# Optimization experiments

Hardware: AMD Instinct MI355X
Metric: run time of the kernel (lower is better)

## Reference

```python
import jax, jax.numpy as jnp
import numpy as np

N = 50000
E = 500000
IN_DIM = 128
HID = 128
EDGE_DIM = 1
MAX_DEPTH = 4  # depth values in [0, MAX_DEPTH]


def setup_inputs() -> dict:
    key = jax.random.key(0)
    ks = jax.random.split(key, 10)
    x = jax.random.normal(ks[0], (N, IN_DIM), jnp.float32)
    edge_index = jax.random.randint(ks[1], (2, E), 0, N)
    edge_attr = jax.random.normal(ks[2], (E, EDGE_DIM), jnp.float32)
    depth = jax.random.randint(ks[3], (N,), 0, MAX_DEPTH + 1)
    def w(k, sh):
        return (jax.random.normal(k, sh, jnp.float32) / np.float32(np.sqrt(sh[0])))
    return {
        "x": x, "edge_index": edge_index, "edge_attr": edge_attr, "depth": depth,
        "pw": w(ks[4], (IN_DIM, HID)), "pb": jnp.zeros((HID,), jnp.float32),
        "mw1": w(ks[5], (HID + EDGE_DIM, HID)), "mb1": jnp.zeros((HID,), jnp.float32),
        "mw2": w(ks[6], (HID, HID)), "mb2": jnp.zeros((HID,), jnp.float32),
        "uw1": w(ks[7], (2 * HID, HID)), "ub1": jnp.zeros((HID,), jnp.float32),
        "uw2": w(ks[8], (HID, HID)), "ub2": jnp.zeros((HID,), jnp.float32),
    }


def reference(x, edge_index, edge_attr, depth, pw, pb, mw1, mb1, mw2, mb2, uw1, ub1, uw2, ub2):
    src, dst = edge_index[0], edge_index[1]
    dst_depth = depth[dst]  # [E]
    h = x @ pw + pb  # node_proj -> [N, HID]
    # Sequential topological DP over depth levels (static unroll, small count).
    for d in range(1, MAX_DEPTH + 1):
        emask = dst_depth == d  # [E]
        # msg_mlp over all edges using current h (lower-depth nodes already updated)
        msg_in = jnp.concatenate([h[src], edge_attr], axis=-1)  # [E, HID+EDGE_DIM]
        msgs = jax.nn.relu(jax.nn.relu(msg_in @ mw1 + mb1) @ mw2 + mb2)
        msgs = jnp.where(emask[:, None], msgs, jnp.zeros((), h.dtype))
        agg = jax.ops.segment_sum(msgs, dst, num_segments=N)  # [N, HID]
        counts = jax.ops.segment_sum(emask.astype(h.dtype), dst, num_segments=N)
        agg = agg / jnp.clip(counts, 1.0)[:, None]  # mean aggregation, clamp(min=1)
        upd_in = jnp.concatenate([h, agg], axis=-1)  # [N, 2*HID]
        h_new = jax.nn.relu(jax.nn.relu(upd_in @ uw1 + ub1) @ uw2 + ub2)
        h = jnp.where((depth == d)[:, None], h_new, h)
    return h
```

## Files before the change

### kernel.cpp

```cpp
#include <hip/hip_runtime.h>

typedef _Float16 f16;
typedef f16 f16x2 __attribute__((ext_vector_type(2)));
typedef f16 f16x8 __attribute__((ext_vector_type(8)));
typedef float f32x4 __attribute__((ext_vector_type(4)));
typedef float f32x2 __attribute__((ext_vector_type(2)));

#define MFMA16(a, b, c) __builtin_amdgcn_mfma_f32_16x16x32_f16((a), (b), (c), 0, 0, 0)

static __device__ __forceinline__ f16x8 cvt8(const float* __restrict__ p) {
    f32x4 p0 = *(const f32x4*)p;
    f32x4 p1 = *(const f32x4*)(p + 4);
    f16x8 a;
    a[0] = (f16)p0[0]; a[1] = (f16)p0[1]; a[2] = (f16)p0[2]; a[3] = (f16)p0[3];
    a[4] = (f16)p1[0]; a[5] = (f16)p1[1]; a[6] = (f16)p1[2]; a[7] = (f16)p1[3];
    return a;
}

__global__ __launch_bounds__(256) void k_prep(
        const float* __restrict__ pw, const float* __restrict__ mw1,
        const float* __restrict__ mw2, const float* __restrict__ uw1,
        const float* __restrict__ uw2,
        f16* __restrict__ pwp, f16* __restrict__ mw1p, f16* __restrict__ mw2p,
        f16* __restrict__ uw1p, f16* __restrict__ uw2p,
        const int* __restrict__ ei, int* __restrict__ degv,
        const int* __restrict__ dep, int* __restrict__ dcnt,
        int4* __restrict__ recs, int CB, int E, int N) {
    __shared__ int lcnt[4];
    __shared__ int lbase[4];
    int b = blockIdx.x;
    int t = threadIdx.x;
    if (b < 48) {
        const float* W; f16* out; int fb;
        if (b < 8)       { W = pw;  out = pwp;  fb = b; }
        else if (b < 16) { W = mw1; out = mw1p; fb = b - 8; }
        else if (b < 24) { W = mw2; out = mw2p; fb = b - 16; }
        else if (b < 40) { W = uw1; out = uw1p; fb = b - 24; }
        else             { W = uw2; out = uw2p; fb = b - 40; }
        int idx = fb * 256 + t;
        int lane = idx & 63;
        int nt = (idx >> 6) & 7;
        int kt = idx >> 9;
        int colx = lane & 15, quad = lane >> 4;
        f16* o = out + (size_t)idx * 8;
        const float* wb = W + (size_t)(kt * 32 + quad * 8) * 128 + nt * 16 + colx;
#pragma unroll
        for (int j = 0; j < 8; j++) o[j] = (f16)wb[(size_t)j * 128];
    } else if (b < 48 + CB) {
        int e = (b - 48) * 256 + t;
        if (e < E) atomicAdd(&degv[ei[E + e]], 1);
    } else {
        if (t < 4) lcnt[t] = 0;
        __syncthreads();
        int v = (b - 48 - CB) * 256 + t;
        int d = (v < N) ? dep[v] : 0;
        int p = -1;
        if (d >= 1 && d <= 4) p = atomicAdd(&lcnt[d - 1], 1);
        __syncthreads();
        if (t < 4) lbase[t] = (lcnt[t] > 0) ? atomicAdd(&dcnt[t], lcnt[t]) : 0;
        __syncthreads();
        if (d >= 1 && d <= 4) recs[(size_t)(d - 1) * N + lbase[d - 1] + p].x = v;
    }
}

__global__ __launch_bounds__(256) void k_mid(
        const int* __restrict__ degv, int* __restrict__ bsum, int SB,
        const float* __restrict__ x, const f16* __restrict__ pwp,
        const f16* __restrict__ mw1p, const float* __restrict__ pb,
        const float* __restrict__ mb1, float* __restrict__ h,
        f16* __restrict__ hh, f16* __restrict__ t, int N) {
    __shared__ __align__(16) f16 lds[4][16 * 136];
    __shared__ int wsum[4];
    int tid = threadIdx.x;
    if ((int)blockIdx.x < SB) {
        int idx = blockIdx.x * 256 + tid;
        int v = (idx < N) ? degv[idx] : 0;
#pragma unroll
        for (int off = 32; off; off >>= 1) v += __shfl_down(v, off, 64);
        if ((tid & 63) == 0) wsum[tid >> 6] = v;
        __syncthreads();
        if (tid == 0) bsum[blockIdx.x] = wsum[0] + wsum[1] + wsum[2] + wsum[3];
        return;
    }
    int lane = tid & 63, w = tid >> 6;
    int colx = lane & 15, quad = lane >> 4;
    int base = ((blockIdx.x - SB) * 4 + w) * 16;
    int arow = base + colx;
    int u = arow < N ? arow : N - 1;

    f32x4 c1[8];
#pragma unroll
    for (int nt = 0; nt < 8; nt++) c1[nt] = (f32x4){0.f, 0.f, 0.f, 0.f};
#pragma unroll
    for (int kt = 0; kt < 4; kt++) {
        f16x8 a = cvt8(x + (size_t)u * 128 + kt * 32 + quad * 8);
#pragma unroll
        for (int nt = 0; nt < 8; nt++) {
            f16x8 b = *(const f16x8*)(pwp + ((size_t)(kt * 8 + nt) * 64 + lane) * 8);
            c1[nt] = MFMA16(a, b, c1[nt]);
        }
    }
#pragma unroll
    for (int nt = 0; nt < 8; nt++) {
        float bias = pb[nt * 16 + colx];
#pragma unroll
        for (int reg = 0; reg < 4; reg++) {
            int row = quad * 4 + reg;
            int node = base + row;
            float v = c1[nt][reg] + bias;
            lds[w][row * 136 + nt * 16 + colx] = (f16)v;
            if (node < N) {
                h[(size_t)node * 128 + nt * 16 + colx] = v;
                hh[(size_t)node * 128 + nt * 16 + colx] = (f16)v;
            }
        }
    }
    f32x4 c2[8];
#pragma unroll
    for (int nt = 0; nt < 8; nt++) c2[nt] = (f32x4){0.f, 0.f, 0.f, 0.f};
#pragma unroll
    for (int kt = 0; kt < 4; kt++) {
        f16x8 a = *(const f16x8*)&lds[w][colx * 136 + kt * 32 + quad * 8];
#pragma unroll
        for (int nt = 0; nt < 8; nt++) {
            f16x8 b = *(const f16x8*)(mw1p + ((size_t)(kt * 8 + nt) * 64 + lane) * 8);
            c2[nt] = MFMA16(a, b, c2[nt]);
        }
    }
#pragma unroll
    for (int nt = 0; nt < 8; nt++) {
        float bias = mb1[nt * 16 + colx];
#pragma unroll
        for (int reg = 0; reg < 4; reg++) {
            int node = base + quad * 4 + reg;
            if (node < N) t[(size_t)node * 128 + nt * 16 + colx] = (f16)(c2[nt][reg] + bias);
        }
    }
}

__global__ __launch_bounds__(256) void k_scanC(const int* __restrict__ degv,
                                               const int* __restrict__ bsum,
                                               int* __restrict__ rowp, int N, int E) {
    __shared__ int lds[256];
    __shared__ int wo[4];
    int b = blockIdx.x, t = threadIdx.x;
    int idx = b * 256 + t;
    int v = (idx < N) ? degv[idx] : 0;
    lds[t] = v;
    __syncthreads();
#pragma unroll
    for (int d = 1; d < 256; d <<= 1) {
        int u = (t >= d) ? lds[t - d] : 0;
        __syncthreads();
        lds[t] += u;
        __syncthreads();
    }
    int off = 0;
    for (int j = t; j < b; j += 256) off += bsum[j];
#pragma unroll
    for (int o = 32; o; o >>= 1) off += __shfl_down(off, o, 64);
    if ((t & 63) == 0) wo[t >> 6] = off;
    __syncthreads();
    int boff = wo[0] + wo[1] + wo[2] + wo[3];
    if (idx < N) rowp[idx] = boff + lds[t] - v;
    if (b == 0 && t == 0) rowp[N] = E;
}

__global__ __launch_bounds__(256) void k_scat(const int* __restrict__ ei,
                                              const float* __restrict__ eattr,
                                              const int* __restrict__ dep,
                                              const int* __restrict__ rowp,
                                              int* __restrict__ cur,
                                              int2* __restrict__ esea,
                                              int4* __restrict__ recs,
                                              const int* __restrict__ dcnt,
                                              int E, int N) {
    int gtid = blockIdx.x * 256 + threadIdx.x;
    int gsz = gridDim.x * 256;
    for (int e = gtid; e < E; e += gsz) {
        int s = ei[e], d = ei[E + e];
        int p = rowp[d] + atomicAdd(&cur[d], 1);
        esea[p] = (int2){s | (dep[s] << 20), __float_as_int(eattr[e])};
    }
    for (int d4 = 0; d4 < 4; d4++) {
        int cnt = dcnt[d4];
        for (int i = gtid; i < cnt; i += gsz) {
            int4* r = &recs[(size_t)d4 * N + i];
            int u = r->x;
            r->y = rowp[u];
            r->z = rowp[u + 1];
        }
    }
}

__global__ __launch_bounds__(512) void k_md(
        const f16* __restrict__ tOrg, f16* __restrict__ tUpd,
        const float* __restrict__ mw1, const float* __restrict__ mb2,
        const f16* __restrict__ mw2p, const int2* __restrict__ esea,
        const int4* __restrict__ recs, const int* __restrict__ dcnt,
        const f16* __restrict__ hh, const f16* __restrict__ uw1p,
        const f16* __restrict__ uw2p, const f16* __restrict__ mw1p,
        const float* __restrict__ ub1, const float* __restrict__ ub2,
        const float* __restrict__ mb1, float* __restrict__ h,
        int dIdx, int N) {
    __shared__ __align__(16) f16 bsm[128 * 128];
    __shared__ __align__(16) f16 tbuf[8][16][136];
    __shared__ __align__(16) f16 pool[16][136];
    __shared__ __align__(16) f16 sout[16][136];
    __shared__ int2 ebuf[8][16];
    __shared__ int ids[16], se0[16], se1[16];
    f16* hbuf = &tbuf[0][0][0];

    const int tid = threadIdx.x;
    const int lane = tid & 63;
    const int w = tid >> 6;
    const int colx = lane & 15, quad = lane >> 4;
    const int cnt = dcnt[dIdx];

    {
        const f16x8* s8 = (const f16x8*)mw2p;
        f16x8* d8 = (f16x8*)bsm;
#pragma unroll
        for (int i = 0; i < 4; i++) d8[i * 512 + tid] = s8[i * 512 + tid];
    }

    const float* w1r = mw1 + 128 * 128;
    f16x8 w1h[4];
#pragma unroll
    for (int kt = 0; kt < 4; kt++) {
        f32x4 q0 = *(const f32x4*)(w1r + kt * 32 + quad * 8);
        f32x4 q1 = *(const f32x4*)(w1r + kt * 32 + quad * 8 + 4);
        w1h[kt][0] = (f16)q0[0]; w1h[kt][1] = (f16)q0[1];
        w1h[kt][2] = (f16)q0[2]; w1h[kt][3] = (f16)q0[3];
        w1h[kt][4] = (f16)q1[0]; w1h[kt][5] = (f16)q1[1];
        w1h[kt][6] = (f16)q1[2]; w1h[kt][7] = (f16)q1[3];
    }
    float mb2v[8];
#pragma unroll
    for (int nt = 0; nt < 8; nt++) mb2v[nt] = mb2[nt * 16 + colx];

    const int b = blockIdx.x, nb = gridDim.x;
    const int s0 = (int)((long long)cnt * b / nb);
    const int s1 = (int)((long long)cnt * (b + 1) / nb);

    auto srow = [&](int sv) -> const f16* {
        const f16* tb = ((unsigned)((sv >> 20) - 1) < (unsigned)dIdx) ? tUpd : tOrg;
        return tb + (size_t)(sv & 0xFFFFF) * 128;
    };

    __syncthreads();

    for (int cs = s0; cs < s1; cs += 16) {
        int cc = s1 - cs; if (cc > 16) cc = 16;
        if (tid < 16) {
            if (tid < cc) {
                int4 r = recs[(size_t)dIdx * N + cs + tid];
                ids[tid] = r.x; se0[tid] = r.y; se1[tid] = r.z;
            } else {
                ids[tid] = 0; se0[tid] = 0; se1[tid] = 0;
            }
        }
        __syncthreads();

        for (int g = 0; g < 2; g++) {
            int maxT = 0;
#pragma unroll
            for (int s = 0; s < 8; s++) {
                int r = g * 8 + s;
                int tc = (se1[r] - se0[r] + 15) >> 4;
                if (tc > maxT) maxT = tc;
            }
            float aggv[8] = {0.f, 0.f, 0.f, 0.f, 0.f, 0.f, 0.f, 0.f};
            for (int rd = 0; rd < maxT; rd++) {
                if (tid < 128) {
                    int s = tid >> 4, j = tid & 15;
                    int r = g * 8 + s;
                    int es = se0[r] + rd * 16 + j;
                    if (es < se1[r]) ebuf[s][j] = esea[es];
                }
                __syncthreads();
#pragma unroll
                for (int it = 0; it < 4; it++) {
                    int task = it * 512 + tid;
                    int row = task >> 4, seg = task & 15;
                    int s = row >> 4, j = row & 15;
                    int r = g * 8 + s;
                    int es = se0[r] + rd * 16 + j;
                    if (es < se1[r]) {
                        int sv = ebuf[s][j].x;
                        *(f16x8*)&tbuf[s][j][seg * 8] =
                            *(const f16x8*)(srow(sv) + seg * 8);
                    }
                }
                __syncthreads();
                {
                    int r = g * 8 + w;
                    int bs = se0[r] + rd * 16;
                    int rem = se1[r] - bs;
                    if (rem > 0) {
                        f16 eah = (f16)__int_as_float(ebuf[w][colx].y);
                        f16x8 afr[4];
#pragma unroll
                        for (int kt = 0; kt < 4; kt++) {
                            f16x8 v = *(const f16x8*)&tbuf[w][colx][kt * 32 + quad * 8];
                            f16x8 o;
#pragma unroll
                            for (int j2 = 0; j2 < 8; j2++) {
                                f16 qv = v[j2] + eah * w1h[kt][j2];
                                o[j2] = qv > (f16)0 ? qv : (f16)0;
                            }
                            afr[kt] = o;
                        }
#pragma unroll
                        for (int nt = 0; nt < 8; nt++) {
                            f32x4 c = (f32x4){0.f, 0.f, 0.f, 0.f};
#pragma unroll
                            for (int kt = 0; kt < 4; kt++) {
                                f16x8 bb = *(const f16x8*)&bsm[((kt * 8 + nt) * 64 + lane) * 8];
                                c = MFMA16(afr[kt], bb, c);
                            }
#pragma unroll
                            for (int reg = 0; reg < 4; reg++)
                                if (quad * 4 + reg < rem)
                                    aggv[nt] += fmaxf(c[reg] + mb2v[nt], 0.f);
                        }
                    }
                }
                __syncthreads();
            }
            {
                int r = g * 8 + w;
                int deg = se1[r] - se0[r];
                float inv = 1.f / (float)(deg > 1 ? deg : 1);
#pragma unroll
                for (int nt = 0; nt < 8; nt++) {
                    float s = aggv[nt];
                    s += __shfl_xor(s, 16, 64);
                    s += __shfl_xor(s, 32, 64);
                    if (quad == 0) pool[r][nt * 16 + colx] = (f16)(s * inv);
                }
            }
        }
        __syncthreads();

        if (tid < 256) {
            int row = tid >> 4, seg = tid & 15;
            *(f16x8*)&hbuf[row * 136 + seg * 8] =
                *(const f16x8*)(hh + (size_t)ids[row] * 128 + seg * 8);
        }
        __syncthreads();

        f32x4 c1 = (f32x4){0.f, 0.f, 0.f, 0.f};
#pragma unroll
        for (int kt = 0; kt < 8; kt++) {
            f16x8 a;
            if (kt < 4)
                a = *(const f16x8*)&hbuf[colx * 136 + kt * 32 + quad * 8];
            else
                a = *(const f16x8*)&pool[colx][(kt - 4) * 32 + quad * 8];
            f16x8 bb = *(const f16x8*)(uw1p + ((size_t)(kt * 8 + w) * 64 + lane) * 8);
            c1 = MFMA16(a, bb, c1);
        }
        {
            float bias = ub1[w * 16 + colx];
#pragma unroll
            for (int reg = 0; reg < 4; reg++) {
                int row = quad * 4 + reg;
                sout[row][w * 16 + colx] = (f16)fmaxf(c1[reg] + bias, 0.f);
            }
        }
        __syncthreads();
        f32x4 c2 = (f32x4){0.f, 0.f, 0.f, 0.f};
#pragma unroll
        for (int kt = 0; kt < 4; kt++) {
            f16x8 a = *(const f16x8*)&sout[colx][kt * 32 + quad * 8];
            f16x8 bb = *(const f16x8*)(uw2p + ((size_t)(kt * 8 + w) * 64 + lane) * 8);
            c2 = MFMA16(a, bb, c2);
        }
        {
            float bias = ub2[w * 16 + colx];
#pragma unroll
            for (int reg = 0; reg < 4; reg++) {
                int row = quad * 4 + reg;
                float v = fmaxf(c2[reg] + bias, 0.f);
                pool[row][w * 16 + colx] = (f16)v;
                if (row < cc)
                    h[(size_t)ids[row] * 128 + w * 16 + colx] = v;
            }
        }
        __syncthreads();
        if (dIdx < 3) {
            f32x4 c3 = (f32x4){0.f, 0.f, 0.f, 0.f};
#pragma unroll
            for (int kt = 0; kt < 4; kt++) {
                f16x8 a = *(const f16x8*)&pool[colx][kt * 32 + quad * 8];
                f16x8 bb = *(const f16x8*)(mw1p + ((size_t)(kt * 8 + w) * 64 + lane) * 8);
                c3 = MFMA16(a, bb, c3);
            }
            float bias = mb1[w * 16 + colx];
#pragma unroll
            for (int reg = 0; reg < 4; reg++) {
                int row = quad * 4 + reg;
                if (row < cc)
                    tUpd[(size_t)ids[row] * 128 + w * 16 + colx] =
                        (f16)(c3[reg] + bias);
            }
        }
        __syncthreads();
    }
}

extern "C" void kernel_launch(void* const* d_in, const int* in_sizes, int n_in,
                              void* d_out, int out_size, void* d_ws, size_t ws_size,
                              hipStream_t stream) {
    const float* x    = (const float*)d_in[0];
    const int*   ei   = (const int*)d_in[1];
    const float* eatt = (const float*)d_in[2];
    const int*   dep  = (const int*)d_in[3];
    const float* pw   = (const float*)d_in[4];
    const float* pb   = (const float*)d_in[5];
    const float* mw1  = (const float*)d_in[6];
    const float* mb1  = (const float*)d_in[7];
    const float* mw2  = (const float*)d_in[8];
    const float* mb2  = (const float*)d_in[9];
    const float* uw1  = (const float*)d_in[10];
    const float* ub1  = (const float*)d_in[11];
    const float* uw2  = (const float*)d_in[12];
    const float* ub2  = (const float*)d_in[13];
    float* h = (float*)d_out;

    int N = in_sizes[3];
    int E = in_sizes[1] / 2;
    int NB = (N + 255) / 256;
    int CB = (E + 255) / 256;

    char* ws = (char*)d_ws;
    size_t o = 0;
    auto alloc = [&](size_t bytes) -> char* {
        char* p = ws + o;
        o += (bytes + 255) & ~(size_t)255;
        return p;
    };
    f16*   t    = (f16*)alloc((size_t)N * 128 * 2);
    f16*   hh   = (f16*)alloc((size_t)N * 128 * 2);
    f16*   tUpd = (f16*)alloc((size_t)N * 128 * 2);
    char*  z0   = (char*)alloc(0);
    int*   degv = (int*)alloc((size_t)N * 4);
    int*   cur  = (int*)alloc((size_t)N * 4);
    int*   dcnt = (int*)alloc(64);
    size_t zbytes = (size_t)((char*)alloc(0) - z0);
    int*   rowp = (int*)alloc((size_t)(N + 1) * 4);
    int*   bsum = (int*)alloc((size_t)NB * 4);
    int2*  esea = (int2*)alloc((size_t)E * 8);
    int4*  recs = (int4*)alloc((size_t)4 * N * 16);
    f16*   pwp  = (f16*)alloc(128 * 128 * 2);
    f16*   mw1p = (f16*)alloc(128 * 128 * 2);
    f16*   mw2p = (f16*)alloc(128 * 128 * 2);
    f16*   uw1p = (f16*)alloc(256 * 128 * 2);
    f16*   uw2p = (f16*)alloc(128 * 128 * 2);

    hipMemsetAsync(z0, 0, zbytes, stream);

    k_prep<<<48 + CB + NB, 256, 0, stream>>>(pw, mw1, mw2, uw1, uw2,
                                             pwp, mw1p, mw2p, uw1p, uw2p,
                                             ei, degv, dep, dcnt, recs, CB, E, N);
    int PB = (N + 63) / 64;
    k_mid<<<NB + PB, 256, 0, stream>>>(degv, bsum, NB, x, pwp, mw1p, pb, mb1,
                                       h, hh, t, N);
    k_scanC<<<NB, 256, 0, stream>>>(degv, bsum, rowp, N, E);
    k_scat<<<CB, 256, 0, stream>>>(ei, eatt, dep, rowp, cur, esea, recs, dcnt, E, N);

    for (int d = 0; d < 4; d++) {
        k_md<<<512, 512, 0, stream>>>(t, tUpd, mw1, mb2, mw2p, esea, recs, dcnt,
                                      hh, uw1p, uw2p, mw1p, ub1, ub2, mb1, h,
                                      d, N);
    }
}
```

Measured before the change: 345.7 us.

## Precompute per-edge first-layer messages via source-ordered CSR before MLP

Adds a source-sorted CSR (out-degree counts, scan, forward edge list) and a new per-level k_msg kernel. For each source node it reads the projected row once and writes the relu(t + ea*w) message for every outgoing edge into a dst-ordered message buffer. The destination CSR is now ordered by depth-sorted node, so each level's edges form a contiguous range. k_md then streams precomputed messages contiguously instead of gathering random source rows and applying the edge-attr FMA itself. The trade is an extra kernel launch per level and a large E×128 f16 scratch buffer written and read each level.

```diff
diff --git a/kernel.cpp b/kernel.cpp
--- a/kernel.cpp
+++ b/kernel.cpp
@@ -17,13 +17,25 @@
     return a;
 }
 
+static __device__ __forceinline__ int sorted_node(int i, const int* __restrict__ dcnt,
+                                                  const int4* __restrict__ recs, int N) {
+    int o1 = dcnt[0], o2 = o1 + dcnt[1], o3 = o2 + dcnt[2], o4 = o3 + dcnt[3];
+    int dI, off;
+    if (i < o1)      { dI = 0; off = 0; }
+    else if (i < o2) { dI = 1; off = o1; }
+    else if (i < o3) { dI = 2; off = o2; }
+    else if (i < o4) { dI = 3; off = o3; }
+    else return -1;
+    return recs[(size_t)dI * N + (i - off)].x;
+}
+
 __global__ __launch_bounds__(256) void k_prep(
         const float* __restrict__ pw, const float* __restrict__ mw1,
         const float* __restrict__ mw2, const float* __restrict__ uw1,
         const float* __restrict__ uw2,
         f16* __restrict__ pwp, f16* __restrict__ mw1p, f16* __restrict__ mw2p,
         f16* __restrict__ uw1p, f16* __restrict__ uw2p,
-        const int* __restrict__ ei, int* __restrict__ degv,
+        const int* __restrict__ ei, int* __restrict__ degv, int* __restrict__ odeg,
         const int* __restrict__ dep, int* __restrict__ dcnt,
         int4* __restrict__ recs, int CB, int E, int N) {
     __shared__ int lcnt[4];
@@ -48,7 +60,10 @@
         for (int j = 0; j < 8; j++) o[j] = (f16)wb[(size_t)j * 128];
     } else if (b < 48 + CB) {
         int e = (b - 48) * 256 + t;
-        if (e < E) atomicAdd(&degv[ei[E + e]], 1);
+        if (e < E) {
+            atomicAdd(&degv[ei[E + e]], 1);
+            atomicAdd(&odeg[ei[e]], 1);
+        }
     } else {
         if (t < 4) lcnt[t] = 0;
         __syncthreads();
@@ -64,7 +79,9 @@
 }
 
 __global__ __launch_bounds__(256) void k_mid(
-        const int* __restrict__ degv, int* __restrict__ bsum, int SB,
+        const int* __restrict__ degv, const int* __restrict__ odeg,
+        const int4* __restrict__ recs, const int* __restrict__ dcnt,
+        int* __restrict__ bsum, int SB,
         const float* __restrict__ x, const f16* __restrict__ pwp,
         const f16* __restrict__ mw1p, const float* __restrict__ pb,
         const float* __restrict__ mb1, float* __restrict__ h,
@@ -72,19 +89,27 @@
     __shared__ __align__(16) f16 lds[4][16 * 136];
     __shared__ int wsum[4];
     int tid = threadIdx.x;
-    if ((int)blockIdx.x < SB) {
-        int idx = blockIdx.x * 256 + tid;
-        int v = (idx < N) ? degv[idx] : 0;
+    if ((int)blockIdx.x < 2 * SB) {
+        int bb = blockIdx.x;
+        int v = 0;
+        if (bb < SB) {
+            int i = bb * 256 + tid;
+            int node = sorted_node(i, dcnt, recs, N);
+            if (node >= 0) v = degv[node];
+        } else {
+            int i = (bb - SB) * 256 + tid;
+            v = (i < N) ? odeg[i] : 0;
+        }
 #pragma unroll
         for (int off = 32; off; off >>= 1) v += __shfl_down(v, off, 64);
         if ((tid & 63) == 0) wsum[tid >> 6] = v;
         __syncthreads();
-        if (tid == 0) bsum[blockIdx.x] = wsum[0] + wsum[1] + wsum[2] + wsum[3];
+        if (tid == 0) bsum[bb] = wsum[0] + wsum[1] + wsum[2] + wsum[3];
         return;
     }
     int lane = tid & 63, w = tid >> 6;
     int colx = lane & 15, quad = lane >> 4;
-    int base = ((blockIdx.x - SB) * 4 + w) * 16;
+    int base = ((blockIdx.x - 2 * SB) * 4 + w) * 16;
     int arow = base + colx;
     int u = arow < N ? arow : N - 1;
 
@@ -138,14 +163,31 @@
     }
 }
 
-__global__ __launch_bounds__(256) void k_scanC(const int* __restrict__ degv,
-                                               const int* __restrict__ bsum,
-                                               int* __restrict__ rowp, int N, int E) {
+__global__ __launch_bounds__(256) void k_scanC(
+        const int* __restrict__ degv, const int* __restrict__ odeg,
+        int4* __restrict__ recs, const int* __restrict__ dcnt,
+        const int* __restrict__ bsum, int* __restrict__ rowp,
+        int* __restrict__ orowp, int NBv, int N, int E) {
     __shared__ int lds[256];
     __shared__ int wo[4];
     int b = blockIdx.x, t = threadIdx.x;
-    int idx = b * 256 + t;
-    int v = (idx < N) ? degv[idx] : 0;
+    bool isSrc = b >= NBv;
+    int i = (isSrc ? b - NBv : b) * 256 + t;
+    int node = -1, dI = -1, joff = 0;
+    int v = 0;
+    if (!isSrc) {
+        int o1 = dcnt[0], o2 = o1 + dcnt[1], o3 = o2 + dcnt[2], o4 = o3 + dcnt[3];
+        if (i < o1)      { dI = 0; joff = 0; }
+        else if (i < o2) { dI = 1; joff = o1; }
+        else if (i < o3) { dI = 2; joff = o2; }
+        else if (i < o4) { dI = 3; joff = o3; }
+        if (dI >= 0) {
+            node = recs[(size_t)dI * N + (i - joff)].x;
+            v = degv[node];
+        }
+    } else {
+        v = (i < N) ? odeg[i] : 0;
+    }
     lds[t] = v;
     __syncthreads();
 #pragma unroll
@@ -156,58 +198,94 @@
         __syncthreads();
     }
     int off = 0;
-    for (int j = t; j < b; j += 256) off += bsum[j];
+    for (int j = (isSrc ? NBv : 0) + t; j < b; j += 256) off += bsum[j];
 #pragma unroll
     for (int o = 32; o; o >>= 1) off += __shfl_down(off, o, 64);
     if ((t & 63) == 0) wo[t >> 6] = off;
     __syncthreads();
     int boff = wo[0] + wo[1] + wo[2] + wo[3];
-    if (idx < N) rowp[idx] = boff + lds[t] - v;
-    if (b == 0 && t == 0) rowp[N] = E;
+    int val = boff + lds[t] - v;
+    if (!isSrc && dI >= 0) {
+        rowp[node] = val;
+        int4* r = &recs[(size_t)dI * N + (i - joff)];
+        r->y = val;
+        r->z = val + v;
+    }
+    if (isSrc && i < N) orowp[i] = val;
+    if (isSrc && b == NBv && t == 0) orowp[N] = E;
 }
 
 __global__ __launch_bounds__(256) void k_scat(const int* __restrict__ ei,
                                               const float* __restrict__ eattr,
                                               const int* __restrict__ dep,
                                               const int* __restrict__ rowp,
+                                              const int* __restrict__ orowp,
                                               int* __restrict__ cur,
-                                              int2* __restrict__ esea,
-                                              int4* __restrict__ recs,
-                                              const int* __restrict__ dcnt,
+                                              int* __restrict__ ocur,
+                                              int2* __restrict__ fwd,
                                               int E, int N) {
     int gtid = blockIdx.x * 256 + threadIdx.x;
     int gsz = gridDim.x * 256;
     for (int e = gtid; e < E; e += gsz) {
-        int s = ei[e], d = ei[E + e];
-        int p = rowp[d] + atomicAdd(&cur[d], 1);
-        esea[p] = (int2){s | (dep[s] << 20), __float_as_int(eattr[e])};
-    }
-    for (int d4 = 0; d4 < 4; d4++) {
-        int cnt = dcnt[d4];
-        for (int i = gtid; i < cnt; i += gsz) {
-            int4* r = &recs[(size_t)d4 * N + i];
-            int u = r->x;
-            r->y = rowp[u];
-            r->z = rowp[u + 1];
+        int s = ei[e], dn = ei[E + e];
+        int dd = dep[dn];
+        int px = -1;
+        if (dd >= 1) {
+            int p = rowp[dn] + atomicAdd(&cur[dn], 1);
+            px = p | (dd << 24);
+        }
+        int q = orowp[s] + atomicAdd(&ocur[s], 1);
+        fwd[q] = (int2){px, __float_as_int(eattr[e])};
+    }
+}
+
+__global__ __launch_bounds__(256) void k_msg(
+        const f16* __restrict__ tOrg, const f16* __restrict__ tUpd,
+        const float* __restrict__ mw1, const int* __restrict__ dep,
+        const int* __restrict__ orowp, const int2* __restrict__ fwd,
+        f16* __restrict__ msgbuf, int dIdx, int N) {
+    const int lane = threadIdx.x & 63;
+    const int gw = blockIdx.x * 4 + (threadIdx.x >> 6);
+    const int nw = gridDim.x * 4;
+    const float* w1r = mw1 + 128 * 128;
+    f32x2 wq = *(const f32x2*)(w1r + lane * 2);
+    f16 w0 = (f16)wq[0], w1 = (f16)wq[1];
+    const int want = dIdx + 1;
+
+    for (int s = gw; s < N; s += nw) {
+        int q0 = orowp[s], q1 = orowp[s + 1];
+        if (q0 == q1) continue;
+        int ds = dep[s];
+        const f16* tb = ((unsigned)(ds - 1) < (unsigned)dIdx) ? tUpd : tOrg;
+        f16x2 tv = *(const f16x2*)(tb + (size_t)s * 128 + lane * 2);
+        for (int q = q0; q < q1; q++) {
+            int2 f = fwd[q];
+            if (f.x >= 0 && (f.x >> 24) == want) {
+                f16 ea = (f16)__int_as_float(f.y);
+                f16 a0 = tv[0] + ea * w0;
+                f16 a1 = tv[1] + ea * w1;
+                a0 = a0 > (f16)0 ? a0 : (f16)0;
+                a1 = a1 > (f16)0 ? a1 : (f16)0;
+                f16x2 a = {a0, a1};
+                *(f16x2*)(msgbuf + (size_t)(f.x & 0xFFFFFF) * 128 + lane * 2) = a;
+            }
         }
     }
 }
 
 __global__ __launch_bounds__(512) void k_md(
-        const f16* __restrict__ tOrg, f16* __restrict__ tUpd,
-        const float* __restrict__ mw1, const float* __restrict__ mb2,
-        const f16* __restrict__ mw2p, const int2* __restrict__ esea,
+        const f16* __restrict__ msgbuf, const float* __restrict__ mb2,
+        const f16* __restrict__ mw2p,
         const int4* __restrict__ recs, const int* __restrict__ dcnt,
         const f16* __restrict__ hh, const f16* __restrict__ uw1p,
         const f16* __restrict__ uw2p, const f16* __restrict__ mw1p,
         const float* __restrict__ ub1, const float* __restrict__ ub2,
         const float* __restrict__ mb1, float* __restrict__ h,
-        int dIdx, int N) {
+        f16* __restrict__ tUpd, int dIdx, int N) {
     __shared__ __align__(16) f16 bsm[128 * 128];
     __shared__ __align__(16) f16 tbuf[8][16][136];
     __shared__ __align__(16) f16 pool[16][136];
     __shared__ __align__(16) f16 sout[16][136];
-    __shared__ int2 ebuf[8][16];
     __shared__ int ids[16], se0[16], se1[16];
     f16* hbuf = &tbuf[0][0][0];
 
@@ -223,18 +301,6 @@
 #pragma unroll
         for (int i = 0; i < 4; i++) d8[i * 512 + tid] = s8[i * 512 + tid];
     }
-
-    const float* w1r = mw1 + 128 * 128;
-    f16x8 w1h[4];
-#pragma unroll
-    for (int kt = 0; kt < 4; kt++) {
-        f32x4 q0 = *(const f32x4*)(w1r + kt * 32 + quad * 8);
-        f32x4 q1 = *(const f32x4*)(w1r + kt * 32 + quad * 8 + 4);
-        w1h[kt][0] = (f16)q0[0]; w1h[kt][1] = (f16)q0[1];
-        w1h[kt][2] = (f16)q0[2]; w1h[kt][3] = (f16)q0[3];
-        w1h[kt][4] = (f16)q1[0]; w1h[kt][5] = (f16)q1[1];
-        w1h[kt][6] = (f16)q1[2]; w1h[kt][7] = (f16)q1[3];
-    }
     float mb2v[8];
 #pragma unroll
     for (int nt = 0; nt < 8; nt++) mb2v[nt] = mb2[nt * 16 + colx];
@@ -242,11 +308,6 @@
     const int b = blockIdx.x, nb = gridDim.x;
     const int s0 = (int)((long long)cnt * b / nb);
     const int s1 = (int)((long long)cnt * (b + 1) / nb);
-
-    auto srow = [&](int sv) -> const f16* {
-        const f16* tb = ((unsigned)((sv >> 20) - 1) < (unsigned)dIdx) ? tUpd : tOrg;
-        return tb + (size_t)(sv & 0xFFFFF) * 128;
-    };
 
     __syncthreads();
 
@@ -272,13 +333,6 @@
             }
             float aggv[8] = {0.f, 0.f, 0.f, 0.f, 0.f, 0.f, 0.f, 0.f};
             for (int rd = 0; rd < maxT; rd++) {
-                if (tid < 128) {
-                    int s = tid >> 4, j = tid & 15;
-                    int r = g * 8 + s;
-                    int es = se0[r] + rd * 16 + j;
-                    if (es < se1[r]) ebuf[s][j] = esea[es];
-                }
-                __syncthreads();
 #pragma unroll
                 for (int it = 0; it < 4; it++) {
                     int task = it * 512 + tid;
@@ -287,9 +341,8 @@
                     int r = g * 8 + s;
                     int es = se0[r] + rd * 16 + j;
                     if (es < se1[r]) {
-                        int sv = ebuf[s][j].x;
                         *(f16x8*)&tbuf[s][j][seg * 8] =
-                            *(const f16x8*)(srow(sv) + seg * 8);
+                            *(const f16x8*)(msgbuf + (size_t)es * 128 + seg * 8);
                     }
                 }
                 __syncthreads();
@@ -298,19 +351,10 @@
                     int bs = se0[r] + rd * 16;
                     int rem = se1[r] - bs;
                     if (rem > 0) {
-                        f16 eah = (f16)__int_as_float(ebuf[w][colx].y);
                         f16x8 afr[4];
 #pragma unroll
-                        for (int kt = 0; kt < 4; kt++) {
-                            f16x8 v = *(const f16x8*)&tbuf[w][colx][kt * 32 + quad * 8];
-                            f16x8 o;
-#pragma unroll
-                            for (int j2 = 0; j2 < 8; j2++) {
-                                f16 qv = v[j2] + eah * w1h[kt][j2];
-                                o[j2] = qv > (f16)0 ? qv : (f16)0;
-                            }
-                            afr[kt] = o;
-                        }
+                        for (int kt = 0; kt < 4; kt++)
+                            afr[kt] = *(const f16x8*)&tbuf[w][colx][kt * 32 + quad * 8];
 #pragma unroll
                         for (int nt = 0; nt < 8; nt++) {
                             f32x4 c = (f32x4){0.f, 0.f, 0.f, 0.f};
@@ -446,33 +490,42 @@
     f16*   tUpd = (f16*)alloc((size_t)N * 128 * 2);
     char*  z0   = (char*)alloc(0);
     int*   degv = (int*)alloc((size_t)N * 4);
+    int*   odeg = (int*)alloc((size_t)N * 4);
     int*   cur  = (int*)alloc((size_t)N * 4);
+    int*   ocur = (int*)alloc((size_t)N * 4);
     int*   dcnt = (int*)alloc(64);
     size_t zbytes = (size_t)((char*)alloc(0) - z0);
-    int*   rowp = (int*)alloc((size_t)(N + 1) * 4);
-    int*   bsum = (int*)alloc((size_t)NB * 4);
-    int2*  esea = (int2*)alloc((size_t)E * 8);
-    int4*  recs = (int4*)alloc((size_t)4 * N * 16);
+    int*   rowp  = (int*)alloc((size_t)(N + 1) * 4);
+    int*   orowp = (int*)alloc((size_t)(N + 1) * 4);
+    int*   bsum  = (int*)alloc((size_t)2 * NB * 4);
+    int2*  fwd   = (int2*)alloc((size_t)E * 8);
+    int4*  recs  = (int4*)alloc((size_t)4 * N * 16);
     f16*   pwp  = (f16*)alloc(128 * 128 * 2);
     f16*   mw1p = (f16*)alloc(128 * 128 * 2);
     f16*   mw2p = (f16*)alloc(128 * 128 * 2);
     f16*   uw1p = (f16*)alloc(256 * 128 * 2);
     f16*   uw2p = (f16*)alloc(128 * 128 * 2);
+    f16*   msgbuf = (f16*)alloc((size_t)E * 128 * 2 + 8192);
 
     hipMemsetAsync(z0, 0, zbytes, stream);
 
     k_prep<<<48 + CB + NB, 256, 0, stream>>>(pw, mw1, mw2, uw1, uw2,
                                              pwp, mw1p, mw2p, uw1p, uw2p,
-                                             ei, degv, dep, dcnt, recs, CB, E, N);
+                                             ei, degv, odeg, dep, dcnt, recs,
+                                             CB, E, N);
     int PB = (N + 63) / 64;
-    k_mid<<<NB + PB, 256, 0, stream>>>(degv, bsum, NB, x, pwp, mw1p, pb, mb1,
-                                       h, hh, t, N);
-    k_scanC<<<NB, 256, 0, stream>>>(degv, bsum, rowp, N, E);
-    k_scat<<<CB, 256, 0, stream>>>(ei, eatt, dep, rowp, cur, esea, recs, dcnt, E, N);
+    k_mid<<<2 * NB + PB, 256, 0, stream>>>(degv, odeg, recs, dcnt, bsum, NB,
+                                           x, pwp, mw1p, pb, mb1, h, hh, t, N);
+    k_scanC<<<2 * NB, 256, 0, stream>>>(degv, odeg, recs, dcnt, bsum,
+                                        rowp, orowp, NB, N, E);
+    k_scat<<<CB, 256, 0, stream>>>(ei, eatt, dep, rowp, orowp, cur, ocur,
+                                   fwd, E, N);
 
     for (int d = 0; d < 4; d++) {
-        k_md<<<512, 512, 0, stream>>>(t, tUpd, mw1, mb2, mw2p, esea, recs, dcnt,
+        k_msg<<<2048, 256, 0, stream>>>(t, tUpd, mw1, dep, orowp, fwd,
+                                        msgbuf, d, N);
+        k_md<<<512, 512, 0, stream>>>(msgbuf, mb2, mw2p, recs, dcnt,
                                       hh, uw1p, uw2p, mw1p, ub1, ub2, mb1, h,
-                                      d, N);
-    }
-}
+                                      tUpd, d, N);
+    }
+}
```

New measurement: 503.5 us. 45.7% more time.
